# Kernel tuning notes

Hardware: AMD Instinct MI355X
Metric: run time of the kernel (lower is better)

The kernel has to match this reference:

```python
import jax, jax.numpy as jnp
import numpy as np

EMBED_DIM = 768
NUM_HEADS = 12
HEAD_DIM = EMBED_DIM // NUM_HEADS


def setup_inputs() -> dict:
    key = jax.random.key(0)
    k1, k2, k3, k4, k5 = jax.random.split(key, 5)
    x_q = jax.random.normal(k1, (8, 1024, EMBED_DIM), dtype=jnp.float32)
    s = 1.0 / np.sqrt(EMBED_DIM)
    qkv_w = jax.random.uniform(k2, (3 * EMBED_DIM, EMBED_DIM), jnp.float32, -s, s)
    qkv_b = jax.random.uniform(k3, (3 * EMBED_DIM,), jnp.float32, -s, s)
    out_w = jax.random.uniform(k4, (EMBED_DIM, EMBED_DIM), jnp.float32, -s, s)
    out_b = jax.random.uniform(k5, (EMBED_DIM,), jnp.float32, -s, s)
    return {"x_q": x_q, "qkv_w": qkv_w, "qkv_b": qkv_b, "out_w": out_w, "out_b": out_b}


def reference(x_q, qkv_w, qkv_b, out_w, out_b):
    b, p, c = x_q.shape
    scaling = HEAD_DIM ** (-0.5)
    # qkv projection: [b, p, 3c]
    qkv = x_q @ qkv_w.T + qkv_b
    qkv = qkv.reshape(b, p, 3, NUM_HEADS, HEAD_DIM)
    q = qkv[:, :, 0].transpose(0, 2, 1, 3) * scaling  # [b, h, p, d]
    k = qkv[:, :, 1].transpose(0, 2, 1, 3)
    v = qkv[:, :, 2].transpose(0, 2, 1, 3)
    attn = jnp.einsum('bhqd,bhkd->bhqk', q, k)
    attn = jax.nn.softmax(attn, axis=-1)
    out = jnp.einsum('bhqk,bhkd->bhqd', attn, v)
    out = out.transpose(0, 2, 1, 3).reshape(b, p, c)
    return out @ out_w.T + out_b
```

## Files before the change

### kernel.cpp

```cpp
#include <hip/hip_runtime.h>
#include <stdint.h>

typedef float  f32x4 __attribute__((ext_vector_type(4)));
typedef int    i32x4 __attribute__((ext_vector_type(4)));
typedef short  bf16x8 __attribute__((ext_vector_type(8)));
typedef unsigned short u16;
typedef unsigned int   u32;

#define DEVINL __device__ __forceinline__

DEVINL u16 f2bf(float f) {
  u32 u = __builtin_bit_cast(u32, f);
  u32 r = u + 0x7fffu + ((u >> 16) & 1u);
  return (u16)(r >> 16);
}

DEVINL u32 cvtpk(float lo, float hi) {
  u32 r;
  asm("v_cvt_pk_bf16_f32 %0, %1, %2" : "=v"(r) : "v"(lo), "v"(hi));
  return r;
}

DEVINL void mfma16(f32x4& d, i32x4 a, i32x4 b) {
  d = __builtin_amdgcn_mfma_f32_16x16x32_bf16(
      __builtin_bit_cast(bf16x8, a), __builtin_bit_cast(bf16x8, b), d, 0, 0, 0);
}

#define GLD16(gp, lp) __builtin_amdgcn_global_load_lds( \
    (__attribute__((address_space(1))) void*)(gp), \
    (__attribute__((address_space(3))) void*)(lp), 16, 0, 0)

__global__ void cvt3_f32_bf16(const float* __restrict__ s0, u16* __restrict__ d0, int n0,
                              const float* __restrict__ s1, u16* __restrict__ d1, int n1,
                              const float* __restrict__ s2, u16* __restrict__ d2, int n2) {
  int i = blockIdx.x * blockDim.x + threadIdx.x;
  int stride = gridDim.x * blockDim.x;
  int nt = n0 + n1 + n2;
  for (; i < nt; i += stride) {
    const float* s; u16* d; int j = i;
    if (j < n0) { s = s0; d = d0; }
    else if ((j -= n0) < n1) { s = s1; d = d1; }
    else { j -= n1; s = s2; d = d2; }
    float4 v = ((const float4*)s)[j];
    ushort4 o;
    o.x = f2bf(v.x); o.y = f2bf(v.y); o.z = f2bf(v.z); o.w = f2bf(v.w);
    ((ushort4*)d)[j] = o;
  }
}

template<int BM, int BN, int FM, int FN, int EPI>
__global__ __launch_bounds__(256) void gemm_bt(
    const u16* __restrict__ A, const u16* __restrict__ Bw,
    int M, int N, const float* __restrict__ bias,
    float* __restrict__ Cf, u16* __restrict__ Qb, u16* __restrict__ Kb, u16* __restrict__ Vtb)
{
  constexpr int BK = 64;
  constexpr int K  = 768;
  constexpr int T  = K / BK;
  constexpr int ABYT = BM * BK * 2;
  constexpr int BBYT = BN * BK * 2;
  __shared__ __align__(16) unsigned char sm[2 * (ABYT + BBYT)];

  const int tid = threadIdx.x;
  const int l   = tid & 63;
  const int wid = tid >> 6;
  const int wm  = wid >> 1, wn = wid & 1;
  const int g4  = l >> 4;
  const int c15 = l & 15;

  const int ntiles = N / BN;
  const int wg  = ntiles * (M / BM);
  const int per = wg >> 3;
  const int tile = ((int)blockIdx.x & 7) * per + ((int)blockIdx.x >> 3);
  const int mbase = (tile / ntiles) * BM;
  const int nbase = (tile % ntiles) * BN;

  auto stage = [&](int buf, int kt) {
    unsigned char* ab = sm + buf * (ABYT + BBYT);
    unsigned char* bb = ab + ABYT;
    #pragma unroll
    for (int c = 0; c < BM / 32; ++c) {
      int ch = c * 256 + tid;
      int row = ch & (BM - 1), pl = ch / BM;
      GLD16(A + (size_t)(mbase + row) * K + kt * BK + pl * 8, ab + ch * 16);
    }
    #pragma unroll
    for (int c = 0; c < BN / 32; ++c) {
      int ch = c * 256 + tid;
      int row = ch & (BN - 1), pl = ch / BN;
      GLD16(Bw + (size_t)(nbase + row) * K + kt * BK + pl * 8, bb + ch * 16);
    }
  };

  f32x4 acc[FM][FN] = {};

  stage(0, 0);
  __syncthreads();

  for (int kt = 0; kt < T; ++kt) {
    int cur = kt & 1;
    if (kt + 1 < T) stage(cur ^ 1, kt + 1);
    unsigned char* ab = sm + cur * (ABYT + BBYT);
    unsigned char* bb = ab + ABYT;
    i32x4 af[FM][2], bf[FN][2];
    #pragma unroll
    for (int mt = 0; mt < FM; ++mt)
      #pragma unroll
      for (int ks = 0; ks < 2; ++ks) {
        int row = wm * (BM / 2) + mt * 16 + c15;
        af[mt][ks] = *(const i32x4*)(ab + ((ks * 4 + g4) * BM + row) * 16);
      }
    #pragma unroll
    for (int nt = 0; nt < FN; ++nt)
      #pragma unroll
      for (int ks = 0; ks < 2; ++ks) {
        int row = wn * (BN / 2) + nt * 16 + c15;
        bf[nt][ks] = *(const i32x4*)(bb + ((ks * 4 + g4) * BN + row) * 16);
      }
    __builtin_amdgcn_s_setprio(1);
    #pragma unroll
    for (int mt = 0; mt < FM; ++mt)
      #pragma unroll
      for (int nt = 0; nt < FN; ++nt)
        #pragma unroll
        for (int ks = 0; ks < 2; ++ks)
          mfma16(acc[mt][nt], af[mt][ks], bf[nt][ks]);
    __builtin_amdgcn_s_setprio(0);
    __syncthreads();
  }

  if constexpr (EPI == 0) {
    #pragma unroll
    for (int nt = 0; nt < FN; ++nt) {
      int n = nbase + wn * (BN / 2) + nt * 16 + c15;
      float bv = bias[n];
      #pragma unroll
      for (int mt = 0; mt < FM; ++mt) {
        int m0 = mbase + wm * (BM / 2) + mt * 16 + g4 * 4;
        float* dst = Cf + (size_t)m0 * N + n;
        #pragma unroll
        for (int j = 0; j < 4; ++j) dst[(size_t)j * N] = acc[mt][nt][j] + bv;
      }
    }
  } else {
    const int which = nbase / 768;
    const int hbase = (nbase - which * 768) >> 6;
    unsigned char* L = sm;

    if (which < 2) {
      const float sc = (which == 0) ? 0.125f : 1.0f;
      #pragma unroll
      for (int nt = 0; nt < FN; ++nt) {
        int nrel = wn * (BN / 2) + nt * 16 + c15;
        float bv = bias[nbase + nrel];
        #pragma unroll
        for (int mt = 0; mt < FM; ++mt) {
          int m0 = wm * (BM / 2) + mt * 16 + g4 * 4;
          #pragma unroll
          for (int j = 0; j < 4; ++j) {
            int m = m0 + j;
            *(u16*)(L + m * 256 + ((nrel * 2) ^ ((m & 7) << 4))) =
                f2bf((acc[mt][nt][j] + bv) * sc);
          }
        }
      }
    } else {
      #pragma unroll
      for (int nt = 0; nt < FN; ++nt) {
        int nrel = wn * (BN / 2) + nt * 16 + c15;
        float bv = bias[nbase + nrel];
        #pragma unroll
        for (int mt = 0; mt < FM; ++mt) {
          int m0 = wm * (BM / 2) + mt * 16 + g4 * 4;
          uint2 uu;
          uu.x = cvtpk(acc[mt][nt][0] + bv, acc[mt][nt][1] + bv);
          uu.y = cvtpk(acc[mt][nt][2] + bv, acc[mt][nt][3] + bv);
          *(uint2*)(L + nrel * 256 + ((m0 * 2) ^ ((nrel & 7) << 4))) = uu;
        }
      }
    }
    __syncthreads();

    const int b  = mbase >> 10;
    const int pb = mbase & 1023;
    #pragma unroll
    for (int k = 0; k < 8; ++k) {
      int chunk = k * 256 + tid;
      int row = chunk >> 4, c = chunk & 15;
      i32x4 vdat = *(const i32x4*)(L + row * 256 + ((c * 16) ^ ((row & 7) << 4)));
      if (which < 2) {
        int h = hbase + (c >> 3), d0 = (c & 7) * 8;
        int bh = b * 12 + h;
        u16* base = (which == 0) ? Qb : Kb;
        *(i32x4*)(base + ((size_t)bh * 1024 + pb + row) * 64 + d0) = vdat;
      } else {
        int h = hbase + (row >> 6), d = row & 63;
        int bh = b * 12 + h;
        *(i32x4*)(Vtb + ((size_t)bh * 64 + d) * 1024 + pb + c * 8) = vdat;
      }
    }
  }
}

__global__ __launch_bounds__(256) void attn_fwd(
    const u16* __restrict__ Qb, const u16* __restrict__ Kb,
    const u16* __restrict__ Vtb, u16* __restrict__ Ob)
{
  __shared__ __align__(16) unsigned char sm[16384 + 4 * 8192];
  const int tid = threadIdx.x;
  const int l = tid & 63, wid = tid >> 6;
  const int g4 = l >> 4, c15 = l & 15;
  const int bid = blockIdx.x;
  const int bh = bid % 96, qt = bid / 96;

  const size_t bhoff = (size_t)bh * (1024 * 64);
  const u16* Qg = Qb + bhoff + (size_t)qt * 128 * 64;
  const u16* Kg = Kb + bhoff;
  const u16* Vg = Vtb + bhoff;

  #pragma unroll
  for (int c = 0; c < 4; ++c) {
    int ch = c * 256 + tid;
    int row = ch & 127, pl = ch >> 7;
    GLD16(Qg + (size_t)row * 64 + pl * 8, sm + ch * 16);
  }

  auto stageKV = [&](int buf, int t) {
    unsigned char* kb_ = sm + 16384 + buf * 8192;
    unsigned char* vb_ = sm + 32768 + buf * 8192;
    #pragma unroll
    for (int c = 0; c < 2; ++c) {
      int ch = c * 256 + tid;
      int row = ch & 63, pl = ch >> 6;
      GLD16(Kg + (size_t)(t * 64 + row) * 64 + pl * 8, kb_ + ch * 16);
      GLD16(Vg + (size_t)row * 1024 + t * 64 + pl * 8, vb_ + ch * 16);
    }
  };

  stageKV(0, 0);
  __syncthreads();

  i32x4 qf[2][2];
  #pragma unroll
  for (int qn = 0; qn < 2; ++qn)
    #pragma unroll
    for (int ks = 0; ks < 2; ++ks) {
      int row = wid * 32 + qn * 16 + c15;
      qf[qn][ks] = *(const i32x4*)(sm + ((ks * 4 + g4) * 128 + row) * 16);
    }
  __syncthreads();

  unsigned char* pw = sm + wid * 4096;

  const i32x4 ones = {0x3F803F80, 0x3F803F80, 0x3F803F80, 0x3F803F80};
  constexpr float LOG2E = 1.44269504f;

  f32x4 ot[4][2] = {};
  f32x4 lacc[2] = {};
  float mrow[2] = {-1e30f, -1e30f};
  float mc[2]   = {-1e30f, -1e30f};

  for (int t = 0; t < 16; ++t) {
    int cur = t & 1;
    if (t + 1 < 16) stageKV(cur ^ 1, t + 1);
    unsigned char* kb_ = sm + 16384 + cur * 8192;
    unsigned char* vb_ = sm + 32768 + cur * 8192;

    f32x4 st[4][2] = {};
    __builtin_amdgcn_s_setprio(1);
    #pragma unroll
    for (int ks = 0; ks < 2; ++ks)
      #pragma unroll
      for (int kmt = 0; kmt < 4; ++kmt) {
        i32x4 ka = *(const i32x4*)(kb_ + ((ks * 4 + g4) * 64 + kmt * 16 + c15) * 16);
        mfma16(st[kmt][0], ka, qf[0][ks]);
        mfma16(st[kmt][1], ka, qf[1][ks]);
      }
    __builtin_amdgcn_s_setprio(0);

    #pragma unroll
    for (int qn = 0; qn < 2; ++qn) {
      float mx = fmaxf(fmaxf(fmaxf(st[0][qn][0], st[0][qn][1]), fmaxf(st[0][qn][2], st[0][qn][3])),
                       fmaxf(fmaxf(st[1][qn][0], st[1][qn][1]), fmaxf(st[1][qn][2], st[1][qn][3])));
      mx = fmaxf(mx,
           fmaxf(fmaxf(fmaxf(st[2][qn][0], st[2][qn][1]), fmaxf(st[2][qn][2], st[2][qn][3])),
                 fmaxf(fmaxf(st[3][qn][0], st[3][qn][1]), fmaxf(st[3][qn][2], st[3][qn][3]))));
      mx = fmaxf(mx, __shfl_xor(mx, 16));
      mx = fmaxf(mx, __shfl_xor(mx, 32));
      if (!__all(mx - mrow[qn] <= 8.0f)) {
        float mnew = fmaxf(mrow[qn], mx);
        float sfq = exp2f((mrow[qn] - mnew) * LOG2E);
        mrow[qn] = mnew;
        mc[qn] = mnew * LOG2E;
        #pragma unroll
        for (int dmt = 0; dmt < 4; ++dmt)
          #pragma unroll
          for (int j = 0; j < 4; ++j) ot[dmt][qn][j] *= sfq;
        lacc[qn][0] *= sfq;
      }
      #pragma unroll
      for (int kmt = 0; kmt < 4; ++kmt) {
        float p0 = exp2f(__builtin_fmaf(st[kmt][qn][0], LOG2E, -mc[qn]));
        float p1 = exp2f(__builtin_fmaf(st[kmt][qn][1], LOG2E, -mc[qn]));
        float p2 = exp2f(__builtin_fmaf(st[kmt][qn][2], LOG2E, -mc[qn]));
        float p3 = exp2f(__builtin_fmaf(st[kmt][qn][3], LOG2E, -mc[qn]));
        int k0 = kmt * 16 + 4 * g4;
        uint2 ww;
        ww.x = cvtpk(p0, p1);
        ww.y = cvtpk(p2, p3);
        *(uint2*)(pw + ((k0 >> 3) * 32 + qn * 16 + c15) * 16 + (k0 & 7) * 2) = ww;
      }
    }

    i32x4 pb[2][2];
    #pragma unroll
    for (int qn = 0; qn < 2; ++qn)
      #pragma unroll
      for (int ks = 0; ks < 2; ++ks)
        pb[qn][ks] = *(const i32x4*)(pw + (((ks * 4 + g4) * 32) + qn * 16 + c15) * 16);

    __builtin_amdgcn_s_setprio(1);
    #pragma unroll
    for (int ks = 0; ks < 2; ++ks) {
      #pragma unroll
      for (int dmt = 0; dmt < 4; ++dmt) {
        i32x4 va = *(const i32x4*)(vb_ + ((ks * 4 + g4) * 64 + dmt * 16 + c15) * 16);
        mfma16(ot[dmt][0], va, pb[0][ks]);
        mfma16(ot[dmt][1], va, pb[1][ks]);
      }
      mfma16(lacc[0], ones, pb[0][ks]);
      mfma16(lacc[1], ones, pb[1][ks]);
    }
    __builtin_amdgcn_s_setprio(0);
    __syncthreads();
  }

  const int b = bh / 12, h = bh % 12;
  #pragma unroll
  for (int qn = 0; qn < 2; ++qn) {
    float inv = 1.0f / lacc[qn][0];
    int q = qt * 128 + wid * 32 + qn * 16 + c15;
    size_t rowoff = ((size_t)(b * 1024 + q) * 12 + h) * 64;
    #pragma unroll
    for (int dmt = 0; dmt < 4; ++dmt) {
      int d0 = dmt * 16 + g4 * 4;
      uint2 uu;
      uu.x = cvtpk(ot[dmt][qn][0] * inv, ot[dmt][qn][1] * inv);
      uu.y = cvtpk(ot[dmt][qn][2] * inv, ot[dmt][qn][3] * inv);
      *(uint2*)(Ob + rowoff + d0) = uu;
    }
  }
}

extern "C" void kernel_launch(void* const* d_in, const int* in_sizes, int n_in,
                              void* d_out, int out_size, void* d_ws, size_t ws_size,
                              hipStream_t stream) {
  const float* x    = (const float*)d_in[0];
  const float* qkvw = (const float*)d_in[1];
  const float* qkvb = (const float*)d_in[2];
  const float* outw = (const float*)d_in[3];
  const float* outb = (const float*)d_in[4];
  float* out = (float*)d_out;

  unsigned char* ws = (unsigned char*)d_ws;
  u16* xb  = (u16*)(ws);
  u16* wqb = (u16*)(ws + 12582912);
  u16* wob = (u16*)(ws + 16121856);
  u16* Qbf = (u16*)(ws + 17301504);
  u16* Kbf = (u16*)(ws + 29884416);
  u16* Vtb = (u16*)(ws + 42467328);
  u16* Ob  = xb;

  cvt3_f32_bf16<<<dim3(2048), dim3(256), 0, stream>>>(
      x, xb, 8192 * 768 / 4, qkvw, wqb, 2304 * 768 / 4, outw, wob, 768 * 768 / 4);

  gemm_bt<128, 128, 4, 4, 1><<<dim3(1152), dim3(256), 0, stream>>>(
      xb, wqb, 8192, 2304, qkvb, nullptr, Qbf, Kbf, Vtb);

  attn_fwd<<<dim3(768), dim3(256), 0, stream>>>(Qbf, Kbf, Vtb, Ob);

  gemm_bt<128, 64, 4, 2, 0><<<dim3(768), dim3(256), 0, stream>>>(
      Ob, wob, 8192, 768, outb, out, nullptr, nullptr, nullptr);
}
```

Before: 172.7 us.

## Fuse fp32-to-bf16 conversion of activations into the QKV GEMM A-tile load

The standalone conversion pass no longer converts the 8192x768 input activations. The QKV GEMM now loads fp32 X directly into registers, converts it to bf16 with packed conversions, and writes it to LDS, with the next tile's global loads issued before the MFMAs. This drops a full write and re-read of the bf16 activation copy. In exchange, the GEMM reads twice the bytes for A, holds extra registers for the staged fp32 data, and does the conversion once per N-tile (18 times per element) instead of once overall.

New measurement: 199.2 us. 15.3% more time.

```diff
diff --git a/kernel.cpp b/kernel.cpp
--- a/kernel.cpp
+++ b/kernel.cpp
@@ -30,17 +30,15 @@
     (__attribute__((address_space(1))) void*)(gp), \
     (__attribute__((address_space(3))) void*)(lp), 16, 0, 0)
 
-__global__ void cvt3_f32_bf16(const float* __restrict__ s0, u16* __restrict__ d0, int n0,
-                              const float* __restrict__ s1, u16* __restrict__ d1, int n1,
-                              const float* __restrict__ s2, u16* __restrict__ d2, int n2) {
+__global__ void cvt2_f32_bf16(const float* __restrict__ s0, u16* __restrict__ d0, int n0,
+                              const float* __restrict__ s1, u16* __restrict__ d1, int n1) {
   int i = blockIdx.x * blockDim.x + threadIdx.x;
   int stride = gridDim.x * blockDim.x;
-  int nt = n0 + n1 + n2;
+  int nt = n0 + n1;
   for (; i < nt; i += stride) {
     const float* s; u16* d; int j = i;
     if (j < n0) { s = s0; d = d0; }
-    else if ((j -= n0) < n1) { s = s1; d = d1; }
-    else { j -= n1; s = s2; d = d2; }
+    else { j -= n0; s = s1; d = d1; }
     float4 v = ((const float4*)s)[j];
     ushort4 o;
     o.x = f2bf(v.x); o.y = f2bf(v.y); o.z = f2bf(v.z); o.w = f2bf(v.w);
@@ -48,11 +46,162 @@
   }
 }
 
-template<int BM, int BN, int FM, int FN, int EPI>
+__global__ __launch_bounds__(256) void gemm_qkv_f32a(
+    const float* __restrict__ X, const u16* __restrict__ Bw,
+    const float* __restrict__ bias,
+    u16* __restrict__ Qb, u16* __restrict__ Kb, u16* __restrict__ Vtb)
+{
+  constexpr int BM = 128, BN = 128, BK = 64, K = 768, T = 12;
+  constexpr int ABYT = BM * BK * 2;
+  constexpr int BBYT = BN * BK * 2;
+  __shared__ __align__(16) unsigned char sm[2 * (ABYT + BBYT)];
+
+  const int tid = threadIdx.x;
+  const int l   = tid & 63;
+  const int wid = tid >> 6;
+  const int wm  = wid >> 1, wn = wid & 1;
+  const int g4  = l >> 4;
+  const int c15 = l & 15;
+
+  constexpr int ntiles = 18;
+  const int tile = ((int)blockIdx.x & 7) * 144 + ((int)blockIdx.x >> 3);
+  const int mbase = (tile / ntiles) * BM;
+  const int nbase = (tile % ntiles) * BN;
+
+  float4 hold[8];
+  auto loadA = [&](int kt) {
+    #pragma unroll
+    for (int c = 0; c < 4; ++c) {
+      int ch = c * 256 + tid;
+      int row = ch & 127, pl = ch >> 7;
+      const float* src = X + (size_t)(mbase + row) * K + kt * BK + pl * 8;
+      hold[2 * c]     = ((const float4*)src)[0];
+      hold[2 * c + 1] = ((const float4*)src)[1];
+    }
+  };
+  auto writeA = [&](int buf) {
+    unsigned char* ab = sm + buf * (ABYT + BBYT);
+    #pragma unroll
+    for (int c = 0; c < 4; ++c) {
+      int ch = c * 256 + tid;
+      i32x4 w;
+      w[0] = (int)cvtpk(hold[2 * c].x,     hold[2 * c].y);
+      w[1] = (int)cvtpk(hold[2 * c].z,     hold[2 * c].w);
+      w[2] = (int)cvtpk(hold[2 * c + 1].x, hold[2 * c + 1].y);
+      w[3] = (int)cvtpk(hold[2 * c + 1].z, hold[2 * c + 1].w);
+      *(i32x4*)(ab + ch * 16) = w;
+    }
+  };
+  auto stageB = [&](int buf, int kt) {
+    unsigned char* bb = sm + buf * (ABYT + BBYT) + ABYT;
+    #pragma unroll
+    for (int c = 0; c < 4; ++c) {
+      int ch = c * 256 + tid;
+      int row = ch & 127, pl = ch >> 7;
+      GLD16(Bw + (size_t)(nbase + row) * K + kt * BK + pl * 8, bb + ch * 16);
+    }
+  };
+
+  f32x4 acc[4][4] = {};
+
+  loadA(0); stageB(0, 0); writeA(0);
+  __syncthreads();
+
+  for (int kt = 0; kt < T; ++kt) {
+    int cur = kt & 1;
+    unsigned char* ab = sm + cur * (ABYT + BBYT);
+    unsigned char* bb = ab + ABYT;
+    i32x4 af[4][2], bf[4][2];
+    #pragma unroll
+    for (int mt = 0; mt < 4; ++mt)
+      #pragma unroll
+      for (int ks = 0; ks < 2; ++ks) {
+        int row = wm * 64 + mt * 16 + c15;
+        af[mt][ks] = *(const i32x4*)(ab + ((ks * 4 + g4) * BM + row) * 16);
+      }
+    #pragma unroll
+    for (int nt = 0; nt < 4; ++nt)
+      #pragma unroll
+      for (int ks = 0; ks < 2; ++ks) {
+        int row = wn * 64 + nt * 16 + c15;
+        bf[nt][ks] = *(const i32x4*)(bb + ((ks * 4 + g4) * BN + row) * 16);
+      }
+    if (kt + 1 < T) { loadA(kt + 1); stageB(cur ^ 1, kt + 1); }
+    __builtin_amdgcn_s_setprio(1);
+    #pragma unroll
+    for (int mt = 0; mt < 4; ++mt)
+      #pragma unroll
+      for (int nt = 0; nt < 4; ++nt)
+        #pragma unroll
+        for (int ks = 0; ks < 2; ++ks)
+          mfma16(acc[mt][nt], af[mt][ks], bf[nt][ks]);
+    __builtin_amdgcn_s_setprio(0);
+    if (kt + 1 < T) writeA(cur ^ 1);
+    __syncthreads();
+  }
+
+  const int which = nbase / 768;
+  const int hbase = (nbase - which * 768) >> 6;
+  unsigned char* L = sm;
+
+  if (which < 2) {
+    const float sc = (which == 0) ? 0.125f : 1.0f;
+    #pragma unroll
+    for (int nt = 0; nt < 4; ++nt) {
+      int nrel = wn * 64 + nt * 16 + c15;
+      float bv = bias[nbase + nrel];
+      #pragma unroll
+      for (int mt = 0; mt < 4; ++mt) {
+        int m0 = wm * 64 + mt * 16 + g4 * 4;
+        #pragma unroll
+        for (int j = 0; j < 4; ++j) {
+          int m = m0 + j;
+          *(u16*)(L + m * 256 + ((nrel * 2) ^ ((m & 7) << 4))) =
+              f2bf((acc[mt][nt][j] + bv) * sc);
+        }
+      }
+    }
+  } else {
+    #pragma unroll
+    for (int nt = 0; nt < 4; ++nt) {
+      int nrel = wn * 64 + nt * 16 + c15;
+      float bv = bias[nbase + nrel];
+      #pragma unroll
+      for (int mt = 0; mt < 4; ++mt) {
+        int m0 = wm * 64 + mt * 16 + g4 * 4;
+        uint2 uu;
+        uu.x = cvtpk(acc[mt][nt][0] + bv, acc[mt][nt][1] + bv);
+        uu.y = cvtpk(acc[mt][nt][2] + bv, acc[mt][nt][3] + bv);
+        *(uint2*)(L + nrel * 256 + ((m0 * 2) ^ ((nrel & 7) << 4))) = uu;
+      }
+    }
+  }
+  __syncthreads();
+
+  const int b  = mbase >> 10;
+  const int pb = mbase & 1023;
+  #pragma unroll
+  for (int k = 0; k < 8; ++k) {
+    int chunk = k * 256 + tid;
+    int row = chunk >> 4, c = chunk & 15;
+    i32x4 vdat = *(const i32x4*)(L + row * 256 + ((c * 16) ^ ((row & 7) << 4)));
+    if (which < 2) {
+      int h = hbase + (c >> 3), d0 = (c & 7) * 8;
+      int bh = b * 12 + h;
+      u16* base = (which == 0) ? Qb : Kb;
+      *(i32x4*)(base + ((size_t)bh * 1024 + pb + row) * 64 + d0) = vdat;
+    } else {
+      int h = hbase + (row >> 6), d = row & 63;
+      int bh = b * 12 + h;
+      *(i32x4*)(Vtb + ((size_t)bh * 64 + d) * 1024 + pb + c * 8) = vdat;
+    }
+  }
+}
+
+template<int BM, int BN, int FM, int FN>
 __global__ __launch_bounds__(256) void gemm_bt(
     const u16* __restrict__ A, const u16* __restrict__ Bw,
-    int M, int N, const float* __restrict__ bias,
-    float* __restrict__ Cf, u16* __restrict__ Qb, u16* __restrict__ Kb, u16* __restrict__ Vtb)
+    int M, int N, const float* __restrict__ bias, float* __restrict__ Cf)
 {
   constexpr int BK = 64;
   constexpr int K  = 768;
@@ -129,75 +278,16 @@
     __syncthreads();
   }
 
-  if constexpr (EPI == 0) {
-    #pragma unroll
-    for (int nt = 0; nt < FN; ++nt) {
-      int n = nbase + wn * (BN / 2) + nt * 16 + c15;
-      float bv = bias[n];
-      #pragma unroll
-      for (int mt = 0; mt < FM; ++mt) {
-        int m0 = mbase + wm * (BM / 2) + mt * 16 + g4 * 4;
-        float* dst = Cf + (size_t)m0 * N + n;
-        #pragma unroll
-        for (int j = 0; j < 4; ++j) dst[(size_t)j * N] = acc[mt][nt][j] + bv;
-      }
-    }
-  } else {
-    const int which = nbase / 768;
-    const int hbase = (nbase - which * 768) >> 6;
-    unsigned char* L = sm;
-
-    if (which < 2) {
-      const float sc = (which == 0) ? 0.125f : 1.0f;
-      #pragma unroll
-      for (int nt = 0; nt < FN; ++nt) {
-        int nrel = wn * (BN / 2) + nt * 16 + c15;
-        float bv = bias[nbase + nrel];
-        #pragma unroll
-        for (int mt = 0; mt < FM; ++mt) {
-          int m0 = wm * (BM / 2) + mt * 16 + g4 * 4;
-          #pragma unroll
-          for (int j = 0; j < 4; ++j) {
-            int m = m0 + j;
-            *(u16*)(L + m * 256 + ((nrel * 2) ^ ((m & 7) << 4))) =
-                f2bf((acc[mt][nt][j] + bv) * sc);
-          }
-        }
-      }
-    } else {
-      #pragma unroll
-      for (int nt = 0; nt < FN; ++nt) {
-        int nrel = wn * (BN / 2) + nt * 16 + c15;
-        float bv = bias[nbase + nrel];
-        #pragma unroll
-        for (int mt = 0; mt < FM; ++mt) {
-          int m0 = wm * (BM / 2) + mt * 16 + g4 * 4;
-          uint2 uu;
-          uu.x = cvtpk(acc[mt][nt][0] + bv, acc[mt][nt][1] + bv);
-          uu.y = cvtpk(acc[mt][nt][2] + bv, acc[mt][nt][3] + bv);
-          *(uint2*)(L + nrel * 256 + ((m0 * 2) ^ ((nrel & 7) << 4))) = uu;
-        }
-      }
-    }
-    __syncthreads();
-
-    const int b  = mbase >> 10;
-    const int pb = mbase & 1023;
-    #pragma unroll
-    for (int k = 0; k < 8; ++k) {
-      int chunk = k * 256 + tid;
-      int row = chunk >> 4, c = chunk & 15;
-      i32x4 vdat = *(const i32x4*)(L + row * 256 + ((c * 16) ^ ((row & 7) << 4)));
-      if (which < 2) {
-        int h = hbase + (c >> 3), d0 = (c & 7) * 8;
-        int bh = b * 12 + h;
-        u16* base = (which == 0) ? Qb : Kb;
-        *(i32x4*)(base + ((size_t)bh * 1024 + pb + row) * 64 + d0) = vdat;
-      } else {
-        int h = hbase + (row >> 6), d = row & 63;
-        int bh = b * 12 + h;
-        *(i32x4*)(Vtb + ((size_t)bh * 64 + d) * 1024 + pb + c * 8) = vdat;
-      }
+  #pragma unroll
+  for (int nt = 0; nt < FN; ++nt) {
+    int n = nbase + wn * (BN / 2) + nt * 16 + c15;
+    float bv = bias[n];
+    #pragma unroll
+    for (int mt = 0; mt < FM; ++mt) {
+      int m0 = mbase + wm * (BM / 2) + mt * 16 + g4 * 4;
+      float* dst = Cf + (size_t)m0 * N + n;
+      #pragma unroll
+      for (int j = 0; j < 4; ++j) dst[(size_t)j * N] = acc[mt][nt][j] + bv;
     }
   }
 }
@@ -363,22 +453,21 @@
   float* out = (float*)d_out;
 
   unsigned char* ws = (unsigned char*)d_ws;
-  u16* xb  = (u16*)(ws);
+  u16* Ob  = (u16*)(ws);
   u16* wqb = (u16*)(ws + 12582912);
   u16* wob = (u16*)(ws + 16121856);
   u16* Qbf = (u16*)(ws + 17301504);
   u16* Kbf = (u16*)(ws + 29884416);
   u16* Vtb = (u16*)(ws + 42467328);
-  u16* Ob  = xb;
-
-  cvt3_f32_bf16<<<dim3(2048), dim3(256), 0, stream>>>(
-      x, xb, 8192 * 768 / 4, qkvw, wqb, 2304 * 768 / 4, outw, wob, 768 * 768 / 4);
-
-  gemm_bt<128, 128, 4, 4, 1><<<dim3(1152), dim3(256), 0, stream>>>(
-      xb, wqb, 8192, 2304, qkvb, nullptr, Qbf, Kbf, Vtb);
+
+  cvt2_f32_bf16<<<dim3(1152), dim3(256), 0, stream>>>(
+      qkvw, wqb, 2304 * 768 / 4, outw, wob, 768 * 768 / 4);
+
+  gemm_qkv_f32a<<<dim3(1152), dim3(256), 0, stream>>>(
+      x, wqb, qkvb, Qbf, Kbf, Vtb);
 
   attn_fwd<<<dim3(768), dim3(256), 0, stream>>>(Qbf, Kbf, Vtb, Ob);
 
-  gemm_bt<128, 64, 4, 2, 0><<<dim3(768), dim3(256), 0, stream>>>(
-      Ob, wob, 8192, 768, outb, out, nullptr, nullptr, nullptr);
-}
+  gemm_bt<128, 64, 4, 2><<<dim3(768), dim3(256), 0, stream>>>(
+      Ob, wob, 8192, 768, outb, out);
+}
```
